# Performance work log

Measured on AMD Instinct MI355X. Metric: run time of the kernel, lower is better.

The kernel has to match this reference:

```python
import jax, jax.numpy as jnp
import numpy as np

B, L, S, H, E, D = 2, 2048, 2048, 8, 64, 64

def setup_inputs() -> dict:
    key = jax.random.key(0)
    kq, kk, kv = jax.random.split(key, 3)
    queries = jax.random.normal(kq, (B, L, H, E), dtype=jnp.float32)
    keys = jax.random.normal(kk, (B, S, H, E), dtype=jnp.float32)
    values = jax.random.normal(kv, (B, S, H, D), dtype=jnp.float32)
    return {"queries": queries, "keys": keys, "values": values}

def reference(queries, keys, values):
    # queries: [B,L,H,E], keys: [B,S,H,E], values: [B,S,H,D]
    E_ = queries.shape[-1]
    scale = 1.0 / jnp.sqrt(jnp.asarray(E_, dtype=queries.dtype))
    # scores: [B,H,L,S]
    scores = jnp.einsum('blhe,bshe->bhls', queries, keys)
    # mask_flag=False, use_relative_pos=False, dropout=0.0 -> identity
    A = jax.nn.softmax(scale * scores, axis=-1)
    # output: [B,L,H,D]
    V = jnp.einsum('bhls,bshd->blhd', A, values)
    return V
```

## Files before the change

### kernel.cpp

```cpp
#include <hip/hip_runtime.h>
#include <hip/hip_bf16.h>


#define SCL2 0.18033688011112042f
#define FIXED_M 64.0f
#define FIXED_ML (FIXED_M * SCL2)

#if __has_builtin(__builtin_amdgcn_exp2f)
#define EXP2(x) __builtin_amdgcn_exp2f(x)
#else
#define EXP2(x) exp2f(x)
#endif

typedef __attribute__((ext_vector_type(8))) short bf16x8;
typedef __attribute__((ext_vector_type(4))) float f32x4;
typedef __attribute__((ext_vector_type(16))) float f32x16;

static constexpr int Bc = 2, Lc = 2048, Sc = 2048, Hc = 8, Ec = 64, Dc = 64;
static constexpr int ELEMS = Bc * Lc * Hc * Ec;

static __device__ __forceinline__ unsigned short bfb(float x) {
  union { __hip_bfloat16 h; unsigned short u; } c;
  c.h = __float2bfloat16(x);
  return c.u;
}
static __device__ __forceinline__ unsigned pkbf(float a, float b) {
  union { __hip_bfloat162 h; unsigned u; } c;
  c.h = __float22bfloat162_rn(make_float2(a, b));
  return c.u;
}
static __device__ __forceinline__ bf16x8 pack4(unsigned w0, unsigned w1,
                                               unsigned w2, unsigned w3) {
  union { unsigned u[4]; bf16x8 v; } c;
  c.u[0] = w0; c.u[1] = w1; c.u[2] = w2; c.u[3] = w3;
  return c.v;
}
static __device__ __forceinline__ void plswap(unsigned a, unsigned b,
                                              unsigned& o0, unsigned& o1, int hi) {
#if __has_builtin(__builtin_amdgcn_permlane32_swap)
  auto r = __builtin_amdgcn_permlane32_swap(a, b, false, false);
  o0 = r[0];
  o1 = r[1];
#else
  unsigned ax = (unsigned)__shfl_xor((int)a, 32);
  unsigned bx = (unsigned)__shfl_xor((int)b, 32);
  o0 = hi ? bx : a;
  o1 = hi ? b : ax;
#endif
}
static __device__ __forceinline__ float cross_half_sum(float x, int hi) {
  unsigned ua, ub;
  plswap(__float_as_uint(x), __float_as_uint(x), ua, ub, hi);
  return __uint_as_float(ua) + __uint_as_float(ub);
}

__global__ __launch_bounds__(256) void prep_qkv_kernel(const float* __restrict__ Q,
                                                       const float* __restrict__ K,
                                                       const float* __restrict__ V,
                                                       __hip_bfloat16* __restrict__ Qf,
                                                       __hip_bfloat16* __restrict__ Kc,
                                                       __hip_bfloat16* __restrict__ Vt) {
  __shared__ __hip_bfloat16 tile[4][64][68];
  if (blockIdx.x < 2048) {
    const bool isK = blockIdx.x >= 1024;
    const float* src = isK ? K : Q;
    __hip_bfloat16* dst = isK ? Kc : Qf;
    int t = (blockIdx.x & 1023) * 256 + threadIdx.x;
    int f = t * 8;
    int e = f & 63;
    int h = (f >> 6) & 7;
    int s = (f >> 9) & 2047;
    int b = f >> 20;
    float4 v0 = *reinterpret_cast<const float4*>(src + f);
    float4 v1 = *reinterpret_cast<const float4*>(src + f + 4);
    int es = e >> 4, hi = (e >> 3) & 1;
    int kb = s >> 5, qi = s & 31;
    int o = ((b << 3) + h) * (Sc * 64) + kb * 2048 + es * 512 + hi * 256 + qi * 8;
    union { ushort u[8]; uint4 q; } pk;
    pk.u[0] = bfb(v0.x); pk.u[1] = bfb(v0.y); pk.u[2] = bfb(v0.z); pk.u[3] = bfb(v0.w);
    pk.u[4] = bfb(v1.x); pk.u[5] = bfb(v1.y); pk.u[6] = bfb(v1.z); pk.u[7] = bfb(v1.w);
    *reinterpret_cast<uint4*>(dst + o) = pk.q;
  } else {
    const int w = threadIdx.x >> 6;
    const int lane = threadIdx.x & 63;
    const int task = (blockIdx.x - 2048) * 4 + w;
    const int st = task & 31;
    const int bh = task >> 5;
    const int s0 = st * 64;
    const int b = bh >> 3, h = bh & 7;
#pragma unroll 4
    for (int j = 0; j < 64; ++j) {
      float v = V[((b * Sc + s0 + j) * Hc + h) * 64 + lane];
      tile[w][j][lane] = __float2bfloat16(v);
    }
    __syncthreads();
    const int qi = lane & 31, hi = lane >> 5;
    __hip_bfloat16* Vb = Vt + bh * (Sc * 64);
#pragma unroll
    for (int kb2 = 0; kb2 < 2; ++kb2)
#pragma unroll
      for (int d0 = 0; d0 < 2; ++d0)
#pragma unroll
        for (int ks = 0; ks < 2; ++ks) {
          union { ushort u[8]; uint4 q; } pk;
#pragma unroll
          for (int j = 0; j < 8; ++j) {
            union { __hip_bfloat16 h; ushort u; } c;
            c.h = tile[w][kb2 * 32 + ks * 16 + hi * 8 + j][d0 * 32 + qi];
            pk.u[j] = c.u;
          }
          int o = ((s0 >> 5) + kb2) * 2048 + d0 * 1024 + ks * 512 + lane * 8;
          *reinterpret_cast<uint4*>(Vb + o) = pk.q;
        }
  }
}

static __device__ __forceinline__ void sm_fixed(f32x16& sc, float& l, int hi,
                                                bf16x8& pb0, bf16x8& pb1) {
#pragma unroll
  for (int r = 0; r < 16; ++r) sc[r] = EXP2(sc[r] * SCL2 - FIXED_ML);
  float r0 = (sc[0] + sc[1]) + (sc[2] + sc[3]);
  float r1 = (sc[4] + sc[5]) + (sc[6] + sc[7]);
  float r2 = (sc[8] + sc[9]) + (sc[10] + sc[11]);
  float r3 = (sc[12] + sc[13]) + (sc[14] + sc[15]);
  l += (r0 + r1) + (r2 + r3);

  unsigned c0, c1, c2, c3, y0, y1, y2, y3;
  c0 = pkbf(sc[0], sc[1]);  c1 = pkbf(sc[4], sc[5]);
  c2 = pkbf(sc[2], sc[3]);  c3 = pkbf(sc[6], sc[7]);
  plswap(c0, c1, y0, y2, hi);
  plswap(c2, c3, y1, y3, hi);
  pb0 = pack4(y0, y1, y2, y3);
  c0 = pkbf(sc[8], sc[9]);   c1 = pkbf(sc[12], sc[13]);
  c2 = pkbf(sc[10], sc[11]); c3 = pkbf(sc[14], sc[15]);
  plswap(c0, c1, y0, y2, hi);
  plswap(c2, c3, y1, y3, hi);
  pb1 = pack4(y0, y1, y2, y3);
}

__global__ __launch_bounds__(256, 2) void attn_kernel(const __hip_bfloat16* __restrict__ Qfr,
                                                      const __hip_bfloat16* __restrict__ Kc,
                                                      const __hip_bfloat16* __restrict__ Vt,
                                                      float* __restrict__ Out) {
  __shared__ float obuf[4][2][16][64];
  __shared__ float mlb[2][4][32];

  const int lid = blockIdx.x;
  const int xcd = lid & 7;
  const int i = lid >> 3;
  const int bh = (xcd << 1) | (i >> 5);
  const int q0 = (i & 31) << 6;
  const int w = threadIdx.x >> 6;
  const int lane = threadIdx.x & 63;
  const int qi = lane & 31;
  const int hi = lane >> 5;
  const int b = bh >> 3, h = bh & 7;

  const __hip_bfloat16* Qh = Qfr + bh * (Lc * 64);
  const __hip_bfloat16* Kh = Kc + bh * (Sc * 64);
  const __hip_bfloat16* Vh = Vt + bh * (Sc * 64);

  bf16x8 qf[2][4];
#pragma unroll
  for (int g = 0; g < 2; ++g)
#pragma unroll
    for (int es = 0; es < 4; ++es)
      qf[g][es] = *reinterpret_cast<const bf16x8*>(
          Qh + ((q0 >> 5) + g) * 2048 + es * 512 + lane * 8);

  f32x16 zero;
#pragma unroll
  for (int r = 0; r < 16; ++r) zero[r] = 0.f;

  f32x16 oa0 = zero, ob0 = zero, oa1 = zero, ob1 = zero;
  float l0 = 0.f, l1 = 0.f;

  for (int t = 0; t < 16; ++t) {
    const int tb = (w + 4 * t) * 2048 + lane * 8;
    const __hip_bfloat16* Kp = Kh + tb;
    bf16x8 k0 = *reinterpret_cast<const bf16x8*>(Kp + 0 * 512);
    bf16x8 k1 = *reinterpret_cast<const bf16x8*>(Kp + 1 * 512);
    bf16x8 k2 = *reinterpret_cast<const bf16x8*>(Kp + 2 * 512);
    bf16x8 k3 = *reinterpret_cast<const bf16x8*>(Kp + 3 * 512);
    const __hip_bfloat16* Vp = Vh + tb;
    bf16x8 v0 = *reinterpret_cast<const bf16x8*>(Vp + 0 * 512);
    bf16x8 v1 = *reinterpret_cast<const bf16x8*>(Vp + 1 * 512);
    bf16x8 v2 = *reinterpret_cast<const bf16x8*>(Vp + 2 * 512);
    bf16x8 v3 = *reinterpret_cast<const bf16x8*>(Vp + 3 * 512);

    f32x16 sc0, sc1;
    __builtin_amdgcn_s_setprio(1);
    sc0 = __builtin_amdgcn_mfma_f32_32x32x16_bf16(k0, qf[0][0], zero, 0, 0, 0);
    sc0 = __builtin_amdgcn_mfma_f32_32x32x16_bf16(k1, qf[0][1], sc0, 0, 0, 0);
    sc0 = __builtin_amdgcn_mfma_f32_32x32x16_bf16(k2, qf[0][2], sc0, 0, 0, 0);
    sc0 = __builtin_amdgcn_mfma_f32_32x32x16_bf16(k3, qf[0][3], sc0, 0, 0, 0);
    sc1 = __builtin_amdgcn_mfma_f32_32x32x16_bf16(k0, qf[1][0], zero, 0, 0, 0);
    sc1 = __builtin_amdgcn_mfma_f32_32x32x16_bf16(k1, qf[1][1], sc1, 0, 0, 0);
    sc1 = __builtin_amdgcn_mfma_f32_32x32x16_bf16(k2, qf[1][2], sc1, 0, 0, 0);
    sc1 = __builtin_amdgcn_mfma_f32_32x32x16_bf16(k3, qf[1][3], sc1, 0, 0, 0);
    __builtin_amdgcn_s_setprio(0);

    bf16x8 pa0, pa1, pb0, pb1;
    sm_fixed(sc0, l0, hi, pa0, pa1);
    sm_fixed(sc1, l1, hi, pb0, pb1);

    __builtin_amdgcn_s_setprio(1);
    oa0 = __builtin_amdgcn_mfma_f32_32x32x16_bf16(v0, pa0, oa0, 0, 0, 0);
    oa1 = __builtin_amdgcn_mfma_f32_32x32x16_bf16(v0, pb0, oa1, 0, 0, 0);
    oa0 = __builtin_amdgcn_mfma_f32_32x32x16_bf16(v1, pa1, oa0, 0, 0, 0);
    oa1 = __builtin_amdgcn_mfma_f32_32x32x16_bf16(v1, pb1, oa1, 0, 0, 0);
    ob0 = __builtin_amdgcn_mfma_f32_32x32x16_bf16(v2, pa0, ob0, 0, 0, 0);
    ob1 = __builtin_amdgcn_mfma_f32_32x32x16_bf16(v2, pb0, ob1, 0, 0, 0);
    ob0 = __builtin_amdgcn_mfma_f32_32x32x16_bf16(v3, pa1, ob0, 0, 0, 0);
    ob1 = __builtin_amdgcn_mfma_f32_32x32x16_bf16(v3, pb1, ob1, 0, 0, 0);
    __builtin_amdgcn_s_setprio(0);
  }

  l0 = cross_half_sum(l0, hi);
  l1 = cross_half_sum(l1, hi);

  if (hi == 0) {
    mlb[0][w][qi] = l0;
    mlb[1][w][qi] = l1;
  }
  __syncthreads();
  float inv[2];
#pragma unroll
  for (int g = 0; g < 2; ++g)
    inv[g] = 1.0f / (mlb[g][0][qi] + mlb[g][1][qi] + mlb[g][2][qi] + mlb[g][3][qi]);

  const int d0 = w >> 1, rr = (w & 1) * 8;
#pragma unroll
  for (int g = 0; g < 2; ++g) {
    if (g) __syncthreads();
    const f32x16& A = g ? oa1 : oa0;
    const f32x16& Bv = g ? ob1 : ob0;
#pragma unroll
    for (int r = 0; r < 16; ++r) {
      obuf[w][0][r][lane] = A[r];
      obuf[w][1][r][lane] = Bv[r];
    }
    __syncthreads();
    float* orow = Out + ((b * Lc + q0 + g * 32 + qi) * Hc + h) * Dc;
#pragma unroll
    for (int t = 0; t < 2; ++t) {
      f32x4 acc;
#pragma unroll
      for (int j = 0; j < 4; ++j) {
        const int r = rr + 4 * t + j;
        acc[j] = (obuf[0][d0][r][lane] + obuf[1][d0][r][lane] +
                  obuf[2][d0][r][lane] + obuf[3][d0][r][lane]) * inv[g];
      }
      const int dbase = d0 * 32 + ((rr + 4 * t) >> 2) * 8 + hi * 4;
      *reinterpret_cast<f32x4*>(orow + dbase) = acc;
    }
  }
}

extern "C" void kernel_launch(void* const* d_in, const int* in_sizes, int n_in,
                              void* d_out, int out_size, void* d_ws, size_t ws_size,
                              hipStream_t stream) {
  const float* Q = (const float*)d_in[0];
  const float* K = (const float*)d_in[1];
  const float* V = (const float*)d_in[2];
  float* out = (float*)d_out;

  __hip_bfloat16* Qf = (__hip_bfloat16*)d_ws;
  __hip_bfloat16* Kc = Qf + ELEMS;
  __hip_bfloat16* Vt = Kc + ELEMS;

  prep_qkv_kernel<<<dim3(2176), 256, 0, stream>>>(Q, K, V, Qf, Kc, Vt);
  attn_kernel<<<dim3(512), 256, 0, stream>>>(Qf, Kc, Vt, out);
}
```

Measured before the change: 40.43 us.

## Split KV sequence across two blocks, load Q directly, merge partials in extra kernel

The attention kernel now splits the key/value range in half across twice as many blocks. Each block writes unnormalized fp16 partial outputs and row sums, and a new merge kernel combines and normalizes them. Q is loaded as fp32 directly in the attention kernel, with the softmax scale folded in before the bf16 conversion, so Q preprocessing is dropped from the prep kernel. The fixed max offset is removed from the exponent. This adds a third launch and extra partial-output traffic in exchange for more parallelism, and removing the fixed offset raises overflow risk.

```diff
diff --git a/kernel.cpp b/kernel.cpp
--- a/kernel.cpp
+++ b/kernel.cpp
@@ -1,10 +1,9 @@
 #include <hip/hip_runtime.h>
 #include <hip/hip_bf16.h>
+#include <hip/hip_fp16.h>
 
 
 #define SCL2 0.18033688011112042f
-#define FIXED_M 64.0f
-#define FIXED_ML (FIXED_M * SCL2)
 
 #if __has_builtin(__builtin_amdgcn_exp2f)
 #define EXP2(x) __builtin_amdgcn_exp2f(x)
@@ -54,36 +53,31 @@
   return __uint_as_float(ua) + __uint_as_float(ub);
 }
 
-__global__ __launch_bounds__(256) void prep_qkv_kernel(const float* __restrict__ Q,
-                                                       const float* __restrict__ K,
-                                                       const float* __restrict__ V,
-                                                       __hip_bfloat16* __restrict__ Qf,
-                                                       __hip_bfloat16* __restrict__ Kc,
-                                                       __hip_bfloat16* __restrict__ Vt) {
+__global__ __launch_bounds__(256) void prep_kv_kernel(const float* __restrict__ K,
+                                                      const float* __restrict__ V,
+                                                      __hip_bfloat16* __restrict__ Kc,
+                                                      __hip_bfloat16* __restrict__ Vt) {
   __shared__ __hip_bfloat16 tile[4][64][68];
-  if (blockIdx.x < 2048) {
-    const bool isK = blockIdx.x >= 1024;
-    const float* src = isK ? K : Q;
-    __hip_bfloat16* dst = isK ? Kc : Qf;
-    int t = (blockIdx.x & 1023) * 256 + threadIdx.x;
+  if (blockIdx.x < 1024) {
+    int t = blockIdx.x * 256 + threadIdx.x;
     int f = t * 8;
     int e = f & 63;
     int h = (f >> 6) & 7;
     int s = (f >> 9) & 2047;
     int b = f >> 20;
-    float4 v0 = *reinterpret_cast<const float4*>(src + f);
-    float4 v1 = *reinterpret_cast<const float4*>(src + f + 4);
+    float4 v0 = *reinterpret_cast<const float4*>(K + f);
+    float4 v1 = *reinterpret_cast<const float4*>(K + f + 4);
     int es = e >> 4, hi = (e >> 3) & 1;
     int kb = s >> 5, qi = s & 31;
     int o = ((b << 3) + h) * (Sc * 64) + kb * 2048 + es * 512 + hi * 256 + qi * 8;
     union { ushort u[8]; uint4 q; } pk;
     pk.u[0] = bfb(v0.x); pk.u[1] = bfb(v0.y); pk.u[2] = bfb(v0.z); pk.u[3] = bfb(v0.w);
     pk.u[4] = bfb(v1.x); pk.u[5] = bfb(v1.y); pk.u[6] = bfb(v1.z); pk.u[7] = bfb(v1.w);
-    *reinterpret_cast<uint4*>(dst + o) = pk.q;
+    *reinterpret_cast<uint4*>(Kc + o) = pk.q;
   } else {
     const int w = threadIdx.x >> 6;
     const int lane = threadIdx.x & 63;
-    const int task = (blockIdx.x - 2048) * 4 + w;
+    const int task = (blockIdx.x - 1024) * 4 + w;
     const int st = task & 31;
     const int bh = task >> 5;
     const int s0 = st * 64;
@@ -118,7 +112,7 @@
 static __device__ __forceinline__ void sm_fixed(f32x16& sc, float& l, int hi,
                                                 bf16x8& pb0, bf16x8& pb1) {
 #pragma unroll
-  for (int r = 0; r < 16; ++r) sc[r] = EXP2(sc[r] * SCL2 - FIXED_ML);
+  for (int r = 0; r < 16; ++r) sc[r] = EXP2(sc[r]);
   float r0 = (sc[0] + sc[1]) + (sc[2] + sc[3]);
   float r1 = (sc[4] + sc[5]) + (sc[6] + sc[7]);
   float r2 = (sc[8] + sc[9]) + (sc[10] + sc[11]);
@@ -138,35 +132,42 @@
   pb1 = pack4(y0, y1, y2, y3);
 }
 
-__global__ __launch_bounds__(256, 2) void attn_kernel(const __hip_bfloat16* __restrict__ Qfr,
+__global__ __launch_bounds__(256, 2) void attn_kernel(const float* __restrict__ Qf32,
                                                       const __hip_bfloat16* __restrict__ Kc,
                                                       const __hip_bfloat16* __restrict__ Vt,
-                                                      float* __restrict__ Out) {
+                                                      __half* __restrict__ Op,
+                                                      float* __restrict__ lp) {
   __shared__ float obuf[4][2][16][64];
   __shared__ float mlb[2][4][32];
 
   const int lid = blockIdx.x;
   const int xcd = lid & 7;
   const int i = lid >> 3;
-  const int bh = (xcd << 1) | (i >> 5);
-  const int q0 = (i & 31) << 6;
+  const int bh = (xcd << 1) | (i >> 6);
+  const int rem = i & 63;
+  const int q0 = (rem >> 1) << 6;
+  const int sh = rem & 1;
   const int w = threadIdx.x >> 6;
   const int lane = threadIdx.x & 63;
   const int qi = lane & 31;
   const int hi = lane >> 5;
   const int b = bh >> 3, h = bh & 7;
 
-  const __hip_bfloat16* Qh = Qfr + bh * (Lc * 64);
   const __hip_bfloat16* Kh = Kc + bh * (Sc * 64);
   const __hip_bfloat16* Vh = Vt + bh * (Sc * 64);
 
   bf16x8 qf[2][4];
 #pragma unroll
-  for (int g = 0; g < 2; ++g)
-#pragma unroll
-    for (int es = 0; es < 4; ++es)
-      qf[g][es] = *reinterpret_cast<const bf16x8*>(
-          Qh + ((q0 >> 5) + g) * 2048 + es * 512 + lane * 8);
+  for (int g = 0; g < 2; ++g) {
+    const float* qrow = Qf32 + ((b * Lc + q0 + g * 32 + qi) * Hc + h) * 64 + hi * 8;
+#pragma unroll
+    for (int es = 0; es < 4; ++es) {
+      float4 a = *reinterpret_cast<const float4*>(qrow + es * 16);
+      float4 c = *reinterpret_cast<const float4*>(qrow + es * 16 + 4);
+      qf[g][es] = pack4(pkbf(a.x * SCL2, a.y * SCL2), pkbf(a.z * SCL2, a.w * SCL2),
+                        pkbf(c.x * SCL2, c.y * SCL2), pkbf(c.z * SCL2, c.w * SCL2));
+    }
+  }
 
   f32x16 zero;
 #pragma unroll
@@ -175,8 +176,8 @@
   f32x16 oa0 = zero, ob0 = zero, oa1 = zero, ob1 = zero;
   float l0 = 0.f, l1 = 0.f;
 
-  for (int t = 0; t < 16; ++t) {
-    const int tb = (w + 4 * t) * 2048 + lane * 8;
+  for (int t = 0; t < 8; ++t) {
+    const int tb = (w + 4 * sh + 8 * t) * 2048 + lane * 8;
     const __hip_bfloat16* Kp = Kh + tb;
     bf16x8 k0 = *reinterpret_cast<const bf16x8*>(Kp + 0 * 512);
     bf16x8 k1 = *reinterpret_cast<const bf16x8*>(Kp + 1 * 512);
@@ -224,10 +225,10 @@
     mlb[1][w][qi] = l1;
   }
   __syncthreads();
-  float inv[2];
-#pragma unroll
-  for (int g = 0; g < 2; ++g)
-    inv[g] = 1.0f / (mlb[g][0][qi] + mlb[g][1][qi] + mlb[g][2][qi] + mlb[g][3][qi]);
+  if (hi == 0 && w < 2) {
+    float Lt = mlb[w][0][qi] + mlb[w][1][qi] + mlb[w][2][qi] + mlb[w][3][qi];
+    lp[sh * 32768 + (b * Lc + q0 + w * 32 + qi) * 8 + h] = Lt;
+  }
 
   const int d0 = w >> 1, rr = (w & 1) * 8;
 #pragma unroll
@@ -241,20 +242,49 @@
       obuf[w][1][r][lane] = Bv[r];
     }
     __syncthreads();
-    float* orow = Out + ((b * Lc + q0 + g * 32 + qi) * Hc + h) * Dc;
+    __half* orow = Op + (size_t)sh * ELEMS + ((b * Lc + q0 + g * 32 + qi) * Hc + h) * Dc;
 #pragma unroll
     for (int t = 0; t < 2; ++t) {
-      f32x4 acc;
-#pragma unroll
-      for (int j = 0; j < 4; ++j) {
-        const int r = rr + 4 * t + j;
-        acc[j] = (obuf[0][d0][r][lane] + obuf[1][d0][r][lane] +
-                  obuf[2][d0][r][lane] + obuf[3][d0][r][lane]) * inv[g];
-      }
+      float s0 = obuf[0][d0][rr + 4 * t + 0][lane] + obuf[1][d0][rr + 4 * t + 0][lane] +
+                 obuf[2][d0][rr + 4 * t + 0][lane] + obuf[3][d0][rr + 4 * t + 0][lane];
+      float s1 = obuf[0][d0][rr + 4 * t + 1][lane] + obuf[1][d0][rr + 4 * t + 1][lane] +
+                 obuf[2][d0][rr + 4 * t + 1][lane] + obuf[3][d0][rr + 4 * t + 1][lane];
+      float s2 = obuf[0][d0][rr + 4 * t + 2][lane] + obuf[1][d0][rr + 4 * t + 2][lane] +
+                 obuf[2][d0][rr + 4 * t + 2][lane] + obuf[3][d0][rr + 4 * t + 2][lane];
+      float s3 = obuf[0][d0][rr + 4 * t + 3][lane] + obuf[1][d0][rr + 4 * t + 3][lane] +
+                 obuf[2][d0][rr + 4 * t + 3][lane] + obuf[3][d0][rr + 4 * t + 3][lane];
+      union { __half2 h[2]; uint2 u; } pk;
+      pk.h[0] = __float22half2_rn(make_float2(s0, s1));
+      pk.h[1] = __float22half2_rn(make_float2(s2, s3));
       const int dbase = d0 * 32 + ((rr + 4 * t) >> 2) * 8 + hi * 4;
-      *reinterpret_cast<f32x4*>(orow + dbase) = acc;
+      *reinterpret_cast<uint2*>(orow + dbase) = pk.u;
     }
   }
+}
+
+__global__ __launch_bounds__(256) void merge_kernel(const __half* __restrict__ Op,
+                                                    const float* __restrict__ lp,
+                                                    float* __restrict__ Out) {
+  int t = blockIdx.x * 256 + threadIdx.x;
+  int f = t * 8;
+  int h = (f >> 6) & 7;
+  int bl = f >> 9;
+  float inv = 1.0f / (lp[bl * 8 + h] + lp[32768 + bl * 8 + h]);
+  union { uint4 q; __half2 hh[4]; } A, B;
+  A.q = *reinterpret_cast<const uint4*>(Op + f);
+  B.q = *reinterpret_cast<const uint4*>(Op + ELEMS + f);
+  f32x4 r0, r1;
+#pragma unroll
+  for (int j = 0; j < 4; ++j) {
+    float2 fa = __half22float2(A.hh[j]);
+    float2 fb = __half22float2(B.hh[j]);
+    float x = (fa.x + fb.x) * inv;
+    float y = (fa.y + fb.y) * inv;
+    if (j < 2) { r0[j * 2] = x; r0[j * 2 + 1] = y; }
+    else       { r1[(j - 2) * 2] = x; r1[(j - 2) * 2 + 1] = y; }
+  }
+  *reinterpret_cast<f32x4*>(Out + f) = r0;
+  *reinterpret_cast<f32x4*>(Out + f + 4) = r1;
 }
 
 extern "C" void kernel_launch(void* const* d_in, const int* in_sizes, int n_in,
@@ -265,10 +295,12 @@
   const float* V = (const float*)d_in[2];
   float* out = (float*)d_out;
 
-  __hip_bfloat16* Qf = (__hip_bfloat16*)d_ws;
-  __hip_bfloat16* Kc = Qf + ELEMS;
+  __hip_bfloat16* Kc = (__hip_bfloat16*)d_ws;
   __hip_bfloat16* Vt = Kc + ELEMS;
-
-  prep_qkv_kernel<<<dim3(2176), 256, 0, stream>>>(Q, K, V, Qf, Kc, Vt);
-  attn_kernel<<<dim3(512), 256, 0, stream>>>(Qf, Kc, Vt, out);
-}
+  __half* Op = (__half*)(Vt + ELEMS);
+  float* lp = (float*)(Op + 2 * (size_t)ELEMS);
+
+  prep_kv_kernel<<<dim3(1152), 256, 0, stream>>>(K, V, Kc, Vt);
+  attn_kernel<<<dim3(1024), 256, 0, stream>>>(Q, Kc, Vt, Op, lp);
+  merge_kernel<<<dim3(1024), 256, 0, stream>>>(Op, lp, out);
+}
```

Measured after the change: 46.96 us. 16.1% more time.
